# Performance work log

Measured on AMD Instinct MI355X. Metric: run time of the kernel, lower is better.

## Reference

```python
import jax, jax.numpy as jnp
import numpy as np

EMBED_DIM = 1024
NUM_HEADS = 16
HEAD_DIM = EMBED_DIM // NUM_HEADS
B, NQ, K = 2, 2048, 2048


def setup_inputs() -> dict:
    key = jax.random.key(0)
    ks = jax.random.split(key, 11)
    s = 1.0 / np.sqrt(EMBED_DIM)
    return {
        "Q_input": jax.random.normal(ks[0], (B, NQ, EMBED_DIM), jnp.float32),
        "K_input": jax.random.normal(ks[1], (B, K, EMBED_DIM), jnp.float32),
        "V_input": jax.random.normal(ks[2], (B, K, EMBED_DIM), jnp.float32),
        "Wq": jax.random.normal(ks[3], (EMBED_DIM, EMBED_DIM), jnp.float32) * s,
        "bq": jnp.zeros((EMBED_DIM,), jnp.float32),
        "Wk": jax.random.normal(ks[4], (EMBED_DIM, EMBED_DIM), jnp.float32) * s,
        "bk": jnp.zeros((EMBED_DIM,), jnp.float32),
        "Wv": jax.random.normal(ks[5], (EMBED_DIM, EMBED_DIM), jnp.float32) * s,
        "bv": jnp.zeros((EMBED_DIM,), jnp.float32),
        "Wo": jax.random.normal(ks[6], (EMBED_DIM, EMBED_DIM), jnp.float32) * s,
        "bo": jnp.zeros((EMBED_DIM,), jnp.float32),
    }


def reference(Q_input, K_input, V_input, Wq, bq, Wk, bk, Wv, bv, Wo, bo):
    b, n_q, _ = Q_input.shape
    k = K_input.shape[1]
    # Linear projections (torch Linear: x @ W.T + b)
    Q = Q_input @ Wq.T + bq
    Kp = K_input @ Wk.T + bk
    V = V_input @ Wv.T + bv
    # [b, h, s, d]
    Q = Q.reshape(b, n_q, NUM_HEADS, HEAD_DIM).transpose(0, 2, 1, 3)
    Kp = Kp.reshape(b, k, NUM_HEADS, HEAD_DIM).transpose(0, 2, 1, 3)
    V = V.reshape(b, k, NUM_HEADS, HEAD_DIM).transpose(0, 2, 1, 3)
    scores = jnp.einsum("bhqd,bhkd->bhqk", Q, Kp) / jnp.sqrt(jnp.float32(HEAD_DIM))
    weights = jax.nn.softmax(scores, axis=-1)
    attn = jnp.einsum("bhqk,bhkd->bhqd", weights, V)
    attn = attn.transpose(0, 2, 1, 3).reshape(b, n_q, EMBED_DIM)
    return attn @ Wo.T + bo
```

## Files before the change

### kernel.cpp

```cpp
#include <hip/hip_runtime.h>
#include <hip/hip_bf16.h>

typedef __bf16  bf16x8 __attribute__((ext_vector_type(8)));
typedef float   f32x4  __attribute__((ext_vector_type(4)));
typedef float   f32x16 __attribute__((ext_vector_type(16)));

#define EMB   1024
#define QSTR  3072
#define HD    64
#define NH    16
#define SEQ   2048
#define BATCH 2
#define TOKENS (BATCH*SEQ)
#define TK    128

typedef __attribute__((address_space(1))) unsigned int* gp_t;
typedef __attribute__((address_space(3))) unsigned int* lp_t;
__device__ __forceinline__ void gload16(const __bf16* g, __bf16* l) {
    __builtin_amdgcn_global_load_lds((gp_t)(unsigned long long)(const void*)g,
                                     (lp_t)(unsigned int)(unsigned long long)(void*)l,
                                     16, 0, 0);
}

__device__ __forceinline__ unsigned int pack2(float a, float b) {
    unsigned short u0 = __builtin_bit_cast(unsigned short, (__bf16)a);
    unsigned short u1 = __builtin_bit_cast(unsigned short, (__bf16)b);
    return (unsigned int)u0 | ((unsigned int)u1 << 16);
}

__global__ __launch_bounds__(256) void cvt4_kernel(
    const float* __restrict__ s0, const float* __restrict__ s1,
    const float* __restrict__ s2, const float* __restrict__ s3,
    __bf16* __restrict__ dst, int n_per)
{
    const float* s = (blockIdx.y == 0) ? s0 : (blockIdx.y == 1) ? s1
                   : (blockIdx.y == 2) ? s2 : s3;
    int i = (blockIdx.x * 256 + threadIdx.x) * 8;
    if (i >= n_per) return;
    float4 a = *(const float4*)(s + i);
    float4 b = *(const float4*)(s + i + 4);
    __bf16 o[8] = {(__bf16)a.x, (__bf16)a.y, (__bf16)a.z, (__bf16)a.w,
                   (__bf16)b.x, (__bf16)b.y, (__bf16)b.z, (__bf16)b.w};
    *(uint4*)(dst + (size_t)blockIdx.y * n_per + i) = *(const uint4*)o;
}

__global__ __launch_bounds__(256, 3) void gemm_qkv(
    const __bf16* __restrict__ X, const __bf16* __restrict__ Wt,
    const float* __restrict__ b0, const float* __restrict__ b1,
    const float* __restrict__ b2, __bf16* __restrict__ Y)
{
    __shared__ __align__(16) __bf16 SMEM[4 * 128 * 32];

    const int tid  = threadIdx.x;
    const int wave = tid >> 6;
    const int lane = tid & 63;
    const int quad = lane >> 4;
    const int l16  = lane & 15;
    const int warp_m = wave >> 1;
    const int warp_n = wave & 1;

    const int bm = blockIdx.y;
    const int bn = blockIdx.x;

    const int lr = lane >> 2;
    const int lc = (lane & 3) ^ ((lr >> 1) & 3);
    const __bf16* Ag = X + (size_t)(bn >> 3) * TOKENS * EMB
                         + (size_t)(bm * 128 + wave * 32 + lr) * EMB + lc * 8;
    const __bf16* Bg = Wt + (size_t)(bn * 128 + wave * 32 + lr) * EMB + lc * 8;
    const int off = wave * 1024;

    f32x4 acc[4][4] = {};

    gload16(Ag,            SMEM + off);
    gload16(Ag + 16 * EMB, SMEM + off + 512);
    gload16(Bg,            SMEM + 8192 + off);
    gload16(Bg + 16 * EMB, SMEM + 8192 + off + 512);

    for (int t = 0; t < EMB / 32; ++t) {
        const int cur = t & 1, nxt = cur ^ 1;
        __syncthreads();
        if (t + 1 < EMB / 32) {
            const __bf16* a0 = Ag + (t + 1) * 32;
            const __bf16* w0 = Bg + (t + 1) * 32;
            gload16(a0,            SMEM + nxt * 4096 + off);
            gload16(a0 + 16 * EMB, SMEM + nxt * 4096 + off + 512);
            gload16(w0,            SMEM + 8192 + nxt * 4096 + off);
            gload16(w0 + 16 * EMB, SMEM + 8192 + nxt * 4096 + off + 512);
        }

        const __bf16* Acur = SMEM + cur * 4096;
        const __bf16* Bcur = SMEM + 8192 + cur * 4096;
        bf16x8 af[4], bf[4];
        #pragma unroll
        for (int i = 0; i < 4; ++i) {
            int rowa = warp_m * 64 + i * 16 + l16;
            int rowb = warp_n * 64 + i * 16 + l16;
            af[i] = *(const bf16x8*)(Acur + (rowa * 4 + (quad ^ ((rowa >> 1) & 3))) * 8);
            bf[i] = *(const bf16x8*)(Bcur + (rowb * 4 + (quad ^ ((rowb >> 1) & 3))) * 8);
        }
        #pragma unroll
        for (int i = 0; i < 4; ++i)
            #pragma unroll
            for (int j = 0; j < 4; ++j)
                acc[i][j] = __builtin_amdgcn_mfma_f32_16x16x32_bf16(af[i], bf[j], acc[i][j], 0, 0, 0);
    }

    if (bn < 16) {
        #pragma unroll
        for (int i = 0; i < 4; ++i)
            #pragma unroll
            for (int j = 0; j < 4; ++j) {
                int n = bn * 128 + warp_n * 64 + j * 16 + l16;
                const float* bsel = (n < 1024) ? b0 : b1;
                float bj = bsel[n & 1023];
                #pragma unroll
                for (int r = 0; r < 4; ++r) {
                    int m = bm * 128 + warp_m * 64 + i * 16 + quad * 4 + r;
                    Y[(size_t)m * QSTR + n] = (__bf16)(acc[i][j][r] + bj);
                }
            }
    } else {
        __bf16* T = SMEM;
        const int b_   = bm >> 4;
        const int tokl = (bm & 15) * 128;
        #pragma unroll
        for (int half = 0; half < 2; ++half) {
            __syncthreads();
            if (warp_m == half) {
                #pragma unroll
                for (int i = 0; i < 4; ++i)
                    #pragma unroll
                    for (int j = 0; j < 4; ++j) {
                        int nl = warp_n * 64 + j * 16 + l16;
                        float bj = b2[(bn & 7) * 128 + nl];
                        #pragma unroll
                        for (int r = 0; r < 4; ++r) {
                            int ml = i * 16 + quad * 4 + r;
                            T[nl * 72 + ml] = (__bf16)(acc[i][j][r] + bj);
                        }
                    }
            }
            __syncthreads();
            {
                const int nl  = tid >> 1;
                const int seg = tid & 1;
                const int hh  = (bn - 16) * 2 + (nl >> 6);
                const int dd  = nl & 63;
                const int tok0 = tokl + half * 64 + seg * 32;
                const int bh_ = b_ * NH + hh;
                __bf16* dst = Y + ((size_t)((bh_ * 64 + dd) * 2 + (tok0 >> 10))) * QSTR
                                + 2048 + (tok0 & 1023);
                #pragma unroll
                for (int k = 0; k < 4; ++k)
                    *(uint4*)(dst + k * 8) = *(const uint4*)&T[nl * 72 + seg * 32 + k * 8];
            }
        }
    }
}

template <typename TY>
__global__ __launch_bounds__(256) void gemm_fast(
    const __bf16* __restrict__ X, const __bf16* __restrict__ Wt,
    const float* __restrict__ b0, TY* __restrict__ Y, int ldy)
{
    __shared__ __align__(16) __bf16 As[2][128 * 64];
    __shared__ __align__(16) __bf16 Bs[2][64 * 64];

    const int tid  = threadIdx.x;
    const int wave = tid >> 6;
    const int lane = tid & 63;
    const int quad = lane >> 4;
    const int l16  = lane & 15;
    const int warp_m = wave >> 1;
    const int warp_n = wave & 1;

    const int bm = blockIdx.y;
    const int bn = blockIdx.x;

    const int lr = lane >> 3;
    const int lc = (lane & 7) ^ lr;
    const __bf16* Ag = X + (size_t)(bm * 128 + wave * 32 + lr) * EMB + lc * 8;
    const __bf16* Bg = Wt + (size_t)(bn * 64 + wave * 16 + lr) * EMB + lc * 8;
    const int aoff = wave * 2048;
    const int boff = wave * 1024;

    f32x4 acc[4][2] = {};

    gload16(Ag,            As[0] + aoff);
    gload16(Ag +  8 * EMB, As[0] + aoff + 512);
    gload16(Ag + 16 * EMB, As[0] + aoff + 1024);
    gload16(Ag + 24 * EMB, As[0] + aoff + 1536);
    gload16(Bg,            Bs[0] + boff);
    gload16(Bg +  8 * EMB, Bs[0] + boff + 512);

    for (int t = 0; t < EMB / 64; ++t) {
        const int cur = t & 1, nxt = cur ^ 1;
        __syncthreads();
        if (t + 1 < EMB / 64) {
            const __bf16* a0 = Ag + (t + 1) * 64;
            const __bf16* w0 = Bg + (t + 1) * 64;
            gload16(a0,            As[nxt] + aoff);
            gload16(a0 +  8 * EMB, As[nxt] + aoff + 512);
            gload16(a0 + 16 * EMB, As[nxt] + aoff + 1024);
            gload16(a0 + 24 * EMB, As[nxt] + aoff + 1536);
            gload16(w0,            Bs[nxt] + boff);
            gload16(w0 +  8 * EMB, Bs[nxt] + boff + 512);
        }

        #pragma unroll
        for (int kk = 0; kk < 2; ++kk) {
            bf16x8 af[4], bf[2];
            #pragma unroll
            for (int i = 0; i < 4; ++i) {
                int row = warp_m * 64 + i * 16 + l16;
                af[i] = *(const bf16x8*)(As[cur] + (row * 8 + ((kk * 4 + quad) ^ (row & 7))) * 8);
            }
            #pragma unroll
            for (int j = 0; j < 2; ++j) {
                int row = warp_n * 32 + j * 16 + l16;
                bf[j] = *(const bf16x8*)(Bs[cur] + (row * 8 + ((kk * 4 + quad) ^ (row & 7))) * 8);
            }
            #pragma unroll
            for (int i = 0; i < 4; ++i)
                #pragma unroll
                for (int j = 0; j < 2; ++j)
                    acc[i][j] = __builtin_amdgcn_mfma_f32_16x16x32_bf16(af[i], bf[j], acc[i][j], 0, 0, 0);
        }
    }

    #pragma unroll
    for (int i = 0; i < 4; ++i)
        #pragma unroll
        for (int j = 0; j < 2; ++j) {
            int n = bn * 64 + warp_n * 32 + j * 16 + l16;
            float bj = b0[n];
            #pragma unroll
            for (int r = 0; r < 4; ++r) {
                int m = bm * 128 + warp_m * 64 + i * 16 + quad * 4 + r;
                Y[(size_t)m * ldy + n] = (TY)(acc[i][j][r] + bj);
            }
        }
}

__global__ __launch_bounds__(256) void attn_kernel(
    const __bf16* __restrict__ QKV, __bf16* __restrict__ Op)
{
    __shared__ __align__(16) __bf16 Ks[2][128 * 64];
    __shared__ __align__(16) __bf16 Vs[2][64 * 128];

    const int tid  = threadIdx.x;
    const int wave = tid >> 6;
    const int lane = tid & 63;
    const int l31  = lane & 31;
    const int hi   = lane >> 5;
    const int e7   = l31 & 7;

    const int qt = blockIdx.x;
    const int h  = blockIdx.y;
    const int b  = blockIdx.z;

    const size_t qoff  = (size_t)b * SEQ * QSTR + (size_t)h * HD;
    const size_t obase = (size_t)b * SEQ * EMB  + (size_t)h * HD;
    const int qbase = qt * 128 + wave * 32;
    const int bh = b * NH + h;

    bf16x8 aq[4];
    {
        const __bf16* qrow = QKV + qoff + (size_t)(qbase + l31) * QSTR + hi * 8;
        #pragma unroll
        for (int dc = 0; dc < 4; ++dc) {
            bf16x8 v = *(const bf16x8*)(qrow + dc * 16);
            #pragma unroll
            for (int i = 0; i < 8; ++i) v[i] = (__bf16)((float)v[i] * 0.125f);
            aq[dc] = v;
        }
    }

    float  l_run   = 0.f;
    f32x16 oacc[2] = {};

    const int kr = tid >> 3;
    const int kc = ((tid & 7) ^ (kr & 7)) << 3;
    const __bf16* Kg0 = QKV + qoff + EMB + (size_t)kr * QSTR + kc;
    const int vr  = tid >> 4;
    const int vpc = tid & 15;
    const int vlc = (vpc & 8) | ((vpc ^ vr) & 7);
    const __bf16* Vg0 = QKV + ((size_t)(bh * 64 + vr) * 2) * QSTR + 2048 + vlc * 8;

    #define STAGE(buf, kb)                                                        \
        {                                                                         \
            _Pragma("unroll")                                                     \
            for (int i_ = 0; i_ < 4; ++i_)                                        \
                gload16(Kg0 + (size_t)((kb) + i_ * 32) * QSTR,                    \
                        Ks[buf] + i_ * 2048 + tid * 8);                           \
            const size_t vt_ = (size_t)((kb) >> 10) * QSTR + ((kb) & 1023);       \
            _Pragma("unroll")                                                     \
            for (int i_ = 0; i_ < 4; ++i_)                                        \
                gload16(Vg0 + (size_t)i_ * 32 * QSTR + vt_,                       \
                        Vs[buf] + i_ * 2048 + tid * 8);                           \
        }

    STAGE(0, 0);

    for (int t = 0; t < SEQ / TK; ++t) {
        const int cur = t & 1, nxt = cur ^ 1;
        __syncthreads();
        if (t + 1 < SEQ / TK) STAGE(nxt, (t + 1) * TK);

        #pragma unroll
        for (int half = 0; half < 2; ++half) {
            const __bf16* Kh = Ks[cur] + half * 4096;
            const int vco = half * 8;

            f32x16 s[2] = {};
            __builtin_amdgcn_s_setprio(1);
            #pragma unroll
            for (int kt = 0; kt < 2; ++kt)
                #pragma unroll
                for (int dc = 0; dc < 4; ++dc) {
                    bf16x8 kf = *(const bf16x8*)(Kh + (kt * 32 + l31) * 64
                                                 + (((2 * dc + hi) ^ e7) << 3));
                    s[kt] = __builtin_amdgcn_mfma_f32_32x32x16_bf16(kf, aq[dc], s[kt], 0, 0, 0);
                }
            __builtin_amdgcn_s_setprio(0);

            unsigned int pw[2][4][2];
            #pragma unroll
            for (int kt = 0; kt < 2; ++kt)
                #pragma unroll
                for (int bq = 0; bq < 4; ++bq) {
                    float e0 = __expf(s[kt][bq * 4 + 0]);
                    float e1 = __expf(s[kt][bq * 4 + 1]);
                    float e2 = __expf(s[kt][bq * 4 + 2]);
                    float e3 = __expf(s[kt][bq * 4 + 3]);
                    l_run += (e0 + e1) + (e2 + e3);
                    pw[kt][bq][0] = pack2(e0, e1);
                    pw[kt][bq][1] = pack2(e2, e3);
                }

            bf16x8 paf[4];
            #pragma unroll
            for (int kt = 0; kt < 2; ++kt)
                #pragma unroll
                for (int m = 0; m < 2; ++m) {
                    unsigned x0 = pw[kt][2 * m][0],     x1 = pw[kt][2 * m][1];
                    unsigned y0 = pw[kt][2 * m + 1][0], y1 = pw[kt][2 * m + 1][1];
                    unsigned px0 = __shfl_xor(x0, 32, 64), px1 = __shfl_xor(x1, 32, 64);
                    unsigned py0 = __shfl_xor(y0, 32, 64), py1 = __shfl_xor(y1, 32, 64);
                    uint4 fw;
                    fw.x = hi ? py0 : x0;
                    fw.y = hi ? py1 : x1;
                    fw.z = hi ? y0  : px0;
                    fw.w = hi ? y1  : px1;
                    paf[kt * 2 + m] = __builtin_bit_cast(bf16x8, fw);
                }

            __builtin_amdgcn_s_setprio(1);
            #pragma unroll
            for (int dh = 0; dh < 2; ++dh)
                #pragma unroll
                for (int ks = 0; ks < 4; ++ks) {
                    bf16x8 bvf = *(const bf16x8*)(Vs[cur] + (dh * 32 + l31) * 128
                                                  + ((vco + ((2 * ks + hi) ^ e7)) << 3));
                    oacc[dh] = __builtin_amdgcn_mfma_f32_32x32x16_bf16(paf[ks], bvf, oacc[dh], 0, 0, 0);
                }
            __builtin_amdgcn_s_setprio(0);
        }
    }

    float lf = l_run + __shfl_xor(l_run, 32, 64);

    #pragma unroll
    for (int r = 0; r < 16; ++r) {
        int qr = (r & 3) + 8 * (r >> 2) + 4 * hi;
        float lq = __shfl(lf, qr, 64);
        #pragma unroll
        for (int dh = 0; dh < 2; ++dh)
            Op[obase + (size_t)(qbase + qr) * EMB + dh * 32 + l31] =
                (__bf16)(oacc[dh][r] / lq);
    }
    #undef STAGE
}

extern "C" void kernel_launch(void* const* d_in, const int* in_sizes, int n_in,
                              void* d_out, int out_size, void* d_ws, size_t ws_size,
                              hipStream_t stream) {
    const float* Qin = (const float*)d_in[0];
    const float* Kin = (const float*)d_in[1];
    const float* Vin = (const float*)d_in[2];
    const float* Wq  = (const float*)d_in[3];
    const float* bq  = (const float*)d_in[4];
    const float* Wk  = (const float*)d_in[5];
    const float* bk  = (const float*)d_in[6];
    const float* Wv  = (const float*)d_in[7];
    const float* bv  = (const float*)d_in[8];
    const float* Wo  = (const float*)d_in[9];
    const float* bo  = (const float*)d_in[10];

    const size_t TENS = (size_t)TOKENS * EMB;
    const size_t WEL  = (size_t)EMB * EMB;
    __bf16* ws = (__bf16*)d_ws;
    __bf16* Xin  = ws;
    __bf16* Wb   = ws + 3 * TENS;
    __bf16* QKVp = ws + 3 * TENS + 4 * WEL;
    __bf16* Ap   = ws;

    cvt4_kernel<<<dim3((unsigned)(TENS / 2048), 3), 256, 0, stream>>>(
        Qin, Kin, Vin, Vin, Xin, (int)TENS);
    cvt4_kernel<<<dim3((unsigned)(WEL / 2048), 4), 256, 0, stream>>>(
        Wq, Wk, Wv, Wo, Wb, (int)WEL);

    gemm_qkv<<<dim3(QSTR / 128, TOKENS / 128), 256, 0, stream>>>(
        Xin, Wb, bq, bk, bv, QKVp);

    attn_kernel<<<dim3(SEQ / 128, NH, BATCH), 256, 0, stream>>>(QKVp, Ap);

    gemm_fast<float><<<dim3(EMB / 64, TOKENS / 128), 256, 0, stream>>>(
        Ap, Wb + 3 * WEL, bo, (float*)d_out, EMB);
}
```

Baseline: 229.5 us.

## Switch attention K/V staging to 3-stage 64-key ring buffer with vmcnt waits

The attention kernel moves from a double-buffered 128-key tile to a triple-buffered 64-key tile ring, prefetching two tiles ahead. The block-wide __syncthreads is replaced with an explicit s_waitcnt vmcnt plus s_barrier, so older loads can complete while newer ones are still in flight. The V layout in LDS is reorganised into 64-wide rows with a matching XOR swizzle. This aims to keep more global loads in flight and hide load latency. The cost is a barrier every 64 keys rather than every 128, and correctness depends on the hand-counted vmcnt value.

```diff
diff --git a/kernel.cpp b/kernel.cpp
--- a/kernel.cpp
+++ b/kernel.cpp
@@ -12,7 +12,7 @@
 #define SEQ   2048
 #define BATCH 2
 #define TOKENS (BATCH*SEQ)
-#define TK    128
+#define TK    64
 
 typedef __attribute__((address_space(1))) unsigned int* gp_t;
 typedef __attribute__((address_space(3))) unsigned int* lp_t;
@@ -245,8 +245,8 @@
 __global__ __launch_bounds__(256) void attn_kernel(
     const __bf16* __restrict__ QKV, __bf16* __restrict__ Op)
 {
-    __shared__ __align__(16) __bf16 Ks[2][128 * 64];
-    __shared__ __align__(16) __bf16 Vs[2][64 * 128];
+    __shared__ __align__(16) __bf16 Ks[3 * 64 * 64];
+    __shared__ __align__(16) __bf16 Vs[3 * 64 * 64];
 
     const int tid  = threadIdx.x;
     const int wave = tid >> 6;
@@ -282,90 +282,91 @@
     const int kr = tid >> 3;
     const int kc = ((tid & 7) ^ (kr & 7)) << 3;
     const __bf16* Kg0 = QKV + qoff + EMB + (size_t)kr * QSTR + kc;
-    const int vr  = tid >> 4;
-    const int vpc = tid & 15;
-    const int vlc = (vpc & 8) | ((vpc ^ vr) & 7);
-    const __bf16* Vg0 = QKV + ((size_t)(bh * 64 + vr) * 2) * QSTR + 2048 + vlc * 8;
-
-    #define STAGE(buf, kb)                                                        \
+    const int vr  = tid >> 3;
+    const int vcl = ((tid & 7) ^ (vr & 7)) << 3;
+    const __bf16* Vg0 = QKV + ((size_t)(bh * 64 + vr) * 2) * QSTR + 2048 + vcl;
+
+    #define STAGE(bufi, kb)                                                       \
         {                                                                         \
-            _Pragma("unroll")                                                     \
-            for (int i_ = 0; i_ < 4; ++i_)                                        \
-                gload16(Kg0 + (size_t)((kb) + i_ * 32) * QSTR,                    \
-                        Ks[buf] + i_ * 2048 + tid * 8);                           \
+            gload16(Kg0 + (size_t)(kb) * QSTR,        Ks + (bufi) * 4096 + tid * 8);        \
+            gload16(Kg0 + (size_t)((kb) + 32) * QSTR, Ks + (bufi) * 4096 + 2048 + tid * 8); \
             const size_t vt_ = (size_t)((kb) >> 10) * QSTR + ((kb) & 1023);       \
-            _Pragma("unroll")                                                     \
-            for (int i_ = 0; i_ < 4; ++i_)                                        \
-                gload16(Vg0 + (size_t)i_ * 32 * QSTR + vt_,                       \
-                        Vs[buf] + i_ * 2048 + tid * 8);                           \
+            gload16(Vg0 + vt_,             Vs + (bufi) * 4096 + tid * 8);         \
+            gload16(Vg0 + 64 * QSTR + vt_, Vs + (bufi) * 4096 + 2048 + tid * 8);  \
         }
 
     STAGE(0, 0);
-
+    STAGE(1, TK);
+
+    int cur = 0;
     for (int t = 0; t < SEQ / TK; ++t) {
-        const int cur = t & 1, nxt = cur ^ 1;
-        __syncthreads();
-        if (t + 1 < SEQ / TK) STAGE(nxt, (t + 1) * TK);
-
-        #pragma unroll
-        for (int half = 0; half < 2; ++half) {
-            const __bf16* Kh = Ks[cur] + half * 4096;
-            const int vco = half * 8;
-
-            f32x16 s[2] = {};
-            __builtin_amdgcn_s_setprio(1);
-            #pragma unroll
-            for (int kt = 0; kt < 2; ++kt)
-                #pragma unroll
-                for (int dc = 0; dc < 4; ++dc) {
-                    bf16x8 kf = *(const bf16x8*)(Kh + (kt * 32 + l31) * 64
-                                                 + (((2 * dc + hi) ^ e7) << 3));
-                    s[kt] = __builtin_amdgcn_mfma_f32_32x32x16_bf16(kf, aq[dc], s[kt], 0, 0, 0);
-                }
-            __builtin_amdgcn_s_setprio(0);
-
-            unsigned int pw[2][4][2];
-            #pragma unroll
-            for (int kt = 0; kt < 2; ++kt)
-                #pragma unroll
-                for (int bq = 0; bq < 4; ++bq) {
-                    float e0 = __expf(s[kt][bq * 4 + 0]);
-                    float e1 = __expf(s[kt][bq * 4 + 1]);
-                    float e2 = __expf(s[kt][bq * 4 + 2]);
-                    float e3 = __expf(s[kt][bq * 4 + 3]);
-                    l_run += (e0 + e1) + (e2 + e3);
-                    pw[kt][bq][0] = pack2(e0, e1);
-                    pw[kt][bq][1] = pack2(e2, e3);
-                }
-
-            bf16x8 paf[4];
-            #pragma unroll
-            for (int kt = 0; kt < 2; ++kt)
-                #pragma unroll
-                for (int m = 0; m < 2; ++m) {
-                    unsigned x0 = pw[kt][2 * m][0],     x1 = pw[kt][2 * m][1];
-                    unsigned y0 = pw[kt][2 * m + 1][0], y1 = pw[kt][2 * m + 1][1];
-                    unsigned px0 = __shfl_xor(x0, 32, 64), px1 = __shfl_xor(x1, 32, 64);
-                    unsigned py0 = __shfl_xor(y0, 32, 64), py1 = __shfl_xor(y1, 32, 64);
-                    uint4 fw;
-                    fw.x = hi ? py0 : x0;
-                    fw.y = hi ? py1 : x1;
-                    fw.z = hi ? y0  : px0;
-                    fw.w = hi ? y1  : px1;
-                    paf[kt * 2 + m] = __builtin_bit_cast(bf16x8, fw);
-                }
-
-            __builtin_amdgcn_s_setprio(1);
-            #pragma unroll
-            for (int dh = 0; dh < 2; ++dh)
-                #pragma unroll
-                for (int ks = 0; ks < 4; ++ks) {
-                    bf16x8 bvf = *(const bf16x8*)(Vs[cur] + (dh * 32 + l31) * 128
-                                                  + ((vco + ((2 * ks + hi) ^ e7)) << 3));
-                    oacc[dh] = __builtin_amdgcn_mfma_f32_32x32x16_bf16(paf[ks], bvf, oacc[dh], 0, 0, 0);
-                }
-            __builtin_amdgcn_s_setprio(0);
-        }
+        if (t < SEQ / TK - 1) asm volatile("s_waitcnt vmcnt(4)" ::: "memory");
+        else                  asm volatile("s_waitcnt vmcnt(0)" ::: "memory");
+        __builtin_amdgcn_s_barrier();
+        __builtin_amdgcn_sched_barrier(0);
+        if (t + 2 < SEQ / TK) {
+            int nb = cur + 2; if (nb >= 3) nb -= 3;
+            STAGE(nb, (t + 2) * TK);
+        }
+
+        const __bf16* Kc = Ks + cur * 4096;
+        const __bf16* Vc = Vs + cur * 4096;
+
+        f32x16 s[2] = {};
+        __builtin_amdgcn_s_setprio(1);
+        #pragma unroll
+        for (int kt = 0; kt < 2; ++kt)
+            #pragma unroll
+            for (int dc = 0; dc < 4; ++dc) {
+                bf16x8 kf = *(const bf16x8*)(Kc + (kt * 32 + l31) * 64
+                                             + (((2 * dc + hi) ^ e7) << 3));
+                s[kt] = __builtin_amdgcn_mfma_f32_32x32x16_bf16(kf, aq[dc], s[kt], 0, 0, 0);
+            }
+        __builtin_amdgcn_s_setprio(0);
+
+        unsigned int pw[2][4][2];
+        #pragma unroll
+        for (int kt = 0; kt < 2; ++kt)
+            #pragma unroll
+            for (int bq = 0; bq < 4; ++bq) {
+                float e0 = __expf(s[kt][bq * 4 + 0]);
+                float e1 = __expf(s[kt][bq * 4 + 1]);
+                float e2 = __expf(s[kt][bq * 4 + 2]);
+                float e3 = __expf(s[kt][bq * 4 + 3]);
+                l_run += (e0 + e1) + (e2 + e3);
+                pw[kt][bq][0] = pack2(e0, e1);
+                pw[kt][bq][1] = pack2(e2, e3);
+            }
+
+        bf16x8 paf[4];
+        #pragma unroll
+        for (int kt = 0; kt < 2; ++kt)
+            #pragma unroll
+            for (int m = 0; m < 2; ++m) {
+                unsigned x0 = pw[kt][2 * m][0],     x1 = pw[kt][2 * m][1];
+                unsigned y0 = pw[kt][2 * m + 1][0], y1 = pw[kt][2 * m + 1][1];
+                unsigned px0 = __shfl_xor(x0, 32, 64), px1 = __shfl_xor(x1, 32, 64);
+                unsigned py0 = __shfl_xor(y0, 32, 64), py1 = __shfl_xor(y1, 32, 64);
+                uint4 fw;
+                fw.x = hi ? py0 : x0;
+                fw.y = hi ? py1 : x1;
+                fw.z = hi ? y0  : px0;
+                fw.w = hi ? y1  : px1;
+                paf[kt * 2 + m] = __builtin_bit_cast(bf16x8, fw);
+            }
+
+        __builtin_amdgcn_s_setprio(1);
+        #pragma unroll
+        for (int dh = 0; dh < 2; ++dh)
+            #pragma unroll
+            for (int ks = 0; ks < 4; ++ks) {
+                bf16x8 bvf = *(const bf16x8*)(Vc + (dh * 32 + l31) * 64
+                                              + (((2 * ks + hi) ^ e7) << 3));
+                oacc[dh] = __builtin_amdgcn_mfma_f32_32x32x16_bf16(paf[ks], bvf, oacc[dh], 0, 0, 0);
+            }
+        __builtin_amdgcn_s_setprio(0);
+
+        cur = (cur == 2) ? 0 : cur + 1;
     }
 
     float lf = l_run + __shfl_xor(l_run, 32, 64);
```

Result: slower. 235.2 us (+2.5%).

## Software-pipeline QK and PV halves with split accumulators in attention loop

Applied to the files above, without the earlier changes.

Restructures the per-tile attention loop so the second half's QK^T MFMAs are issued before the first half's PV MFMAs, interleaving softmax exp work with matrix ops. Uses two independent output accumulators and four partial row-sum registers to break serial dependency chains, then sums them at the end. Drops the s_setprio hints. This raises register pressure, which could lower occupancy or cause spills.

```diff
diff --git a/kernel.cpp b/kernel.cpp
--- a/kernel.cpp
+++ b/kernel.cpp
@@ -276,8 +276,9 @@
         }
     }
 
-    float  l_run   = 0.f;
-    f32x16 oacc[2] = {};
+    float  l4[4] = {};
+    f32x16 oaccA[2] = {};
+    f32x16 oaccB[2] = {};
 
     const int kr = tid >> 3;
     const int kc = ((tid & 7) ^ (kr & 7)) << 3;
@@ -300,6 +301,40 @@
                         Vs[buf] + i_ * 2048 + tid * 8);                           \
         }
 
+    #define SOFTMAX(sreg, paf)                                                    \
+        {                                                                         \
+            unsigned int pw[2][4][2];                                             \
+            _Pragma("unroll")                                                     \
+            for (int kt = 0; kt < 2; ++kt)                                        \
+                _Pragma("unroll")                                                 \
+                for (int bq = 0; bq < 4; ++bq) {                                  \
+                    float e0 = __expf(sreg[kt][bq * 4 + 0]);                      \
+                    float e1 = __expf(sreg[kt][bq * 4 + 1]);                      \
+                    float e2 = __expf(sreg[kt][bq * 4 + 2]);                      \
+                    float e3 = __expf(sreg[kt][bq * 4 + 3]);                      \
+                    l4[(kt * 4 + bq) & 3] += (e0 + e1) + (e2 + e3);               \
+                    pw[kt][bq][0] = pack2(e0, e1);                                \
+                    pw[kt][bq][1] = pack2(e2, e3);                                \
+                }                                                                 \
+            _Pragma("unroll")                                                     \
+            for (int kt = 0; kt < 2; ++kt)                                        \
+                _Pragma("unroll")                                                 \
+                for (int m = 0; m < 2; ++m) {                                     \
+                    unsigned x0 = pw[kt][2 * m][0],     x1 = pw[kt][2 * m][1];    \
+                    unsigned y0 = pw[kt][2 * m + 1][0], y1 = pw[kt][2 * m + 1][1];\
+                    unsigned px0 = __shfl_xor(x0, 32, 64);                        \
+                    unsigned px1 = __shfl_xor(x1, 32, 64);                        \
+                    unsigned py0 = __shfl_xor(y0, 32, 64);                        \
+                    unsigned py1 = __shfl_xor(y1, 32, 64);                        \
+                    uint4 fw;                                                     \
+                    fw.x = hi ? py0 : x0;                                         \
+                    fw.y = hi ? py1 : x1;                                         \
+                    fw.z = hi ? y0  : px0;                                        \
+                    fw.w = hi ? y1  : px1;                                        \
+                    paf[kt * 2 + m] = __builtin_bit_cast(bf16x8, fw);             \
+                }                                                                 \
+        }
+
     STAGE(0, 0);
 
     for (int t = 0; t < SEQ / TK; ++t) {
@@ -307,66 +342,59 @@
         __syncthreads();
         if (t + 1 < SEQ / TK) STAGE(nxt, (t + 1) * TK);
 
-        #pragma unroll
-        for (int half = 0; half < 2; ++half) {
-            const __bf16* Kh = Ks[cur] + half * 4096;
-            const int vco = half * 8;
-
-            f32x16 s[2] = {};
-            __builtin_amdgcn_s_setprio(1);
-            #pragma unroll
-            for (int kt = 0; kt < 2; ++kt)
-                #pragma unroll
-                for (int dc = 0; dc < 4; ++dc) {
-                    bf16x8 kf = *(const bf16x8*)(Kh + (kt * 32 + l31) * 64
-                                                 + (((2 * dc + hi) ^ e7) << 3));
-                    s[kt] = __builtin_amdgcn_mfma_f32_32x32x16_bf16(kf, aq[dc], s[kt], 0, 0, 0);
-                }
-            __builtin_amdgcn_s_setprio(0);
-
-            unsigned int pw[2][4][2];
-            #pragma unroll
-            for (int kt = 0; kt < 2; ++kt)
-                #pragma unroll
-                for (int bq = 0; bq < 4; ++bq) {
-                    float e0 = __expf(s[kt][bq * 4 + 0]);
-                    float e1 = __expf(s[kt][bq * 4 + 1]);
-                    float e2 = __expf(s[kt][bq * 4 + 2]);
-                    float e3 = __expf(s[kt][bq * 4 + 3]);
-                    l_run += (e0 + e1) + (e2 + e3);
-                    pw[kt][bq][0] = pack2(e0, e1);
-                    pw[kt][bq][1] = pack2(e2, e3);
-                }
-
-            bf16x8 paf[4];
-            #pragma unroll
-            for (int kt = 0; kt < 2; ++kt)
-                #pragma unroll
-                for (int m = 0; m < 2; ++m) {
-                    unsigned x0 = pw[kt][2 * m][0],     x1 = pw[kt][2 * m][1];
-                    unsigned y0 = pw[kt][2 * m + 1][0], y1 = pw[kt][2 * m + 1][1];
-                    unsigned px0 = __shfl_xor(x0, 32, 64), px1 = __shfl_xor(x1, 32, 64);
-                    unsigned py0 = __shfl_xor(y0, 32, 64), py1 = __shfl_xor(y1, 32, 64);
-                    uint4 fw;
-                    fw.x = hi ? py0 : x0;
-                    fw.y = hi ? py1 : x1;
-                    fw.z = hi ? y0  : px0;
-                    fw.w = hi ? y1  : px1;
-                    paf[kt * 2 + m] = __builtin_bit_cast(bf16x8, fw);
-                }
-
-            __builtin_amdgcn_s_setprio(1);
-            #pragma unroll
-            for (int dh = 0; dh < 2; ++dh)
-                #pragma unroll
-                for (int ks = 0; ks < 4; ++ks) {
-                    bf16x8 bvf = *(const bf16x8*)(Vs[cur] + (dh * 32 + l31) * 128
-                                                  + ((vco + ((2 * ks + hi) ^ e7)) << 3));
-                    oacc[dh] = __builtin_amdgcn_mfma_f32_32x32x16_bf16(paf[ks], bvf, oacc[dh], 0, 0, 0);
-                }
-            __builtin_amdgcn_s_setprio(0);
-        }
-    }
+        const __bf16* K0 = Ks[cur];
+        const __bf16* K1 = Ks[cur] + 4096;
+        const __bf16* Vc = Vs[cur];
+
+        f32x16 sA[2] = {};
+        #pragma unroll
+        for (int kt = 0; kt < 2; ++kt)
+            #pragma unroll
+            for (int dc = 0; dc < 4; ++dc) {
+                bf16x8 kf = *(const bf16x8*)(K0 + (kt * 32 + l31) * 64
+                                             + (((2 * dc + hi) ^ e7) << 3));
+                sA[kt] = __builtin_amdgcn_mfma_f32_32x32x16_bf16(kf, aq[dc], sA[kt], 0, 0, 0);
+            }
+
+        bf16x8 pafA[4];
+        SOFTMAX(sA, pafA)
+
+        f32x16 sB[2] = {};
+        #pragma unroll
+        for (int kt = 0; kt < 2; ++kt)
+            #pragma unroll
+            for (int dc = 0; dc < 4; ++dc) {
+                bf16x8 kf = *(const bf16x8*)(K1 + (kt * 32 + l31) * 64
+                                             + (((2 * dc + hi) ^ e7) << 3));
+                sB[kt] = __builtin_amdgcn_mfma_f32_32x32x16_bf16(kf, aq[dc], sB[kt], 0, 0, 0);
+            }
+
+        #pragma unroll
+        for (int dh = 0; dh < 2; ++dh)
+            #pragma unroll
+            for (int ks = 0; ks < 4; ++ks) {
+                bf16x8 bvf = *(const bf16x8*)(Vc + (dh * 32 + l31) * 128
+                                              + ((0 + ((2 * ks + hi) ^ e7)) << 3));
+                oaccA[dh] = __builtin_amdgcn_mfma_f32_32x32x16_bf16(pafA[ks], bvf, oaccA[dh], 0, 0, 0);
+            }
+
+        bf16x8 pafB[4];
+        SOFTMAX(sB, pafB)
+
+        #pragma unroll
+        for (int dh = 0; dh < 2; ++dh)
+            #pragma unroll
+            for (int ks = 0; ks < 4; ++ks) {
+                bf16x8 bvf = *(const bf16x8*)(Vc + (dh * 32 + l31) * 128
+                                              + ((8 + ((2 * ks + hi) ^ e7)) << 3));
+                oaccB[dh] = __builtin_amdgcn_mfma_f32_32x32x16_bf16(pafB[ks], bvf, oaccB[dh], 0, 0, 0);
+            }
+    }
+
+    f32x16 oacc[2];
+    oacc[0] = oaccA[0] + oaccB[0];
+    oacc[1] = oaccA[1] + oaccB[1];
+    float l_run = (l4[0] + l4[1]) + (l4[2] + l4[3]);
 
     float lf = l_run + __shfl_xor(l_run, 32, 64);
 
@@ -380,6 +408,7 @@
                 (__bf16)(oacc[dh][r] / lq);
     }
     #undef STAGE
+    #undef SOFTMAX
 }
 
 extern "C" void kernel_launch(void* const* d_in, const int* in_sizes, int n_in,
```

Result: no change. 229.5 us (+0.0%).
